# Kernel optimization log

Hardware: AMD Instinct MI355X
Metric: run time of the kernel (lower is better)

The kernel has to match this reference:

```python
import jax, jax.numpy as jnp
import numpy as np

QDEPTH = 8
WIDTH = 64
HEIGHT = 64
WIRES = 12  # ceil(log2(64*64))
BATCH = 1024


def setup_inputs() -> dict:
    key = jax.random.key(0)
    k1, k2 = jax.random.split(key)
    x = jax.random.normal(k1, (BATCH, 1, WIDTH, HEIGHT), dtype=jnp.float32)
    # torch.nn.Parameter(torch.randn(weight_shape) * 0.4)
    weights = jax.random.normal(k2, (QDEPTH, WIRES, 3), dtype=jnp.float32) * 0.4
    return {"x": x, "weights": weights, "reps": 1}


def _rot_matrices(angles):
    # angles: (L, W, 3) -> (L, W, 2, 2) complex64; Rot(phi, theta, omega) = RZ(omega) RY(theta) RZ(phi)
    phi, theta, omega = angles[..., 0], angles[..., 1], angles[..., 2]
    c = jnp.cos(theta * 0.5).astype(jnp.complex64)
    s = jnp.sin(theta * 0.5).astype(jnp.complex64)
    ep = jnp.exp(-0.5j * (phi + omega).astype(jnp.complex64))  # e^{-i(phi+omega)/2}
    em = jnp.exp(-0.5j * (phi - omega).astype(jnp.complex64))  # e^{-i(phi-omega)/2}
    row0 = jnp.stack([ep * c, -jnp.conj(em) * s], axis=-1)
    row1 = jnp.stack([em * s, jnp.conj(ep) * c], axis=-1)
    return jnp.stack([row0, row1], axis=-2)


def _apply_1q(state, U, wire):
    # state: (B, 2, 2, ..., 2); apply 2x2 U on axis wire+1
    ax = wire + 1
    s = jnp.moveaxis(state, ax, -1)
    s = s @ U.T  # out[..., i] = sum_j U[i, j] s[..., j]
    return jnp.moveaxis(s, -1, ax)


def _apply_cnot(state, control, target):
    c, t = control + 1, target + 1
    s0, s1 = jnp.split(state, 2, axis=c)   # control = 0 / 1 halves
    s1 = jnp.flip(s1, axis=t)              # X on target where control = 1
    return jnp.concatenate([s0, s1], axis=c)


def _sel_layer(state, mats_l, r):
    # one StronglyEntanglingLayers layer: Rot on every wire, then CNOT ring of range r
    for w in range(WIRES):
        state = _apply_1q(state, mats_l[w], w)
    for w in range(WIRES):
        state = _apply_cnot(state, w, (w + r) % WIRES)
    return state


def _circuit(state, weights, reps):
    mats = _rot_matrices(jnp.tanh(weights))  # qw_map.tanh applied to raw weights
    for _ in range(reps):
        for l in range(QDEPTH):
            r = (l % (WIRES - 1)) + 1  # PennyLane default ranges
            layer = jax.checkpoint(lambda s, m, _r=r: _sel_layer(s, m, _r))
            state = layer(state, mats[l])
    return state


def reference(x, weights, reps):
    b = x.shape[0]
    v = x.reshape(b, -1)  # (b, 4096)
    norm = jnp.linalg.norm(v, axis=-1, keepdims=True)
    v = (v / norm).astype(jnp.complex64)
    state = v.reshape((b,) + (2,) * WIRES)
    state = _circuit(state, weights, reps)
    out = state.reshape(b, -1) * norm
    return out.reshape(b, 1, WIDTH, HEIGHT)
```

## Files before the change

### kernel.cpp

```cpp
#include <hip/hip_runtime.h>

#define WIRES   12
#define NSTATE  4096
#define QDEPTH  8
#define BLOCK   256
#define PER_T   16

using f2 = __attribute__((ext_vector_type(2))) float;

__device__ __forceinline__ int slotf(int a) { return a + (a >> 4); }

constexpr int colF(int l, int j) {
    int rr = (l % (WIRES - 1)) + 1;
    int v = 1 << j;
    for (int k = WIRES - 1; k >= 0; --k) {
        int bc = 11 - k;
        int bt = 11 - ((k + rr) % WIRES);
        v ^= ((v >> bc) & 1) << bt;
    }
    return v;
}
struct ColsT { int v[QDEPTH][WIRES]; };
constexpr ColsT mkCols() {
    ColsT c{};
    for (int l = 0; l < QDEPTH; ++l)
        for (int j = 0; j < WIRES; ++j) c.v[l][j] = colF(l, j);
    return c;
}
static __device__ const ColsT COLS = mkCols();

__global__ void mats_kernel(const float* __restrict__ wts, f2* __restrict__ mg)
{
    int t = blockIdx.x * blockDim.x + threadIdx.x;
    if (t >= QDEPTH * WIRES) return;
    float phi   = tanhf(wts[t * 3 + 0]);
    float theta = tanhf(wts[t * 3 + 1]);
    float omega = tanhf(wts[t * 3 + 2]);
    float c  = cosf(theta * 0.5f);
    float s  = sinf(theta * 0.5f);
    float a  = 0.5f * (phi + omega);
    float bm = 0.5f * (phi - omega);
    float ca = cosf(a),  sa = sinf(a);
    float cb = cosf(bm), sb = sinf(bm);
    f2* m = mg + t * 8;
    m[0] = f2{ c * ca,  c * ca};
    m[1] = f2{ c * sa, -c * sa};
    m[2] = f2{-s * cb, -s * cb};
    m[3] = f2{ s * sb, -s * sb};
    m[4] = f2{ s * cb,  s * cb};
    m[5] = f2{ s * sb, -s * sb};
    m[6] = f2{ c * ca,  c * ca};
    m[7] = f2{-c * sa,  c * sa};
}

template<int P>
__device__ __forceinline__ void gate(f2 r[PER_T], const f2* __restrict__ m)
{
    const f2 u00r = m[0], u00w = m[1], u01r = m[2], u01w = m[3];
    const f2 u10r = m[4], u10w = m[5], u11r = m[6], u11w = m[7];
    #pragma unroll
    for (int pr = 0; pr < PER_T / 2; pr += 2) {
        const int k0 = ((pr >> P) << (P + 1)) | (pr & ((1 << P) - 1));
        const int k1 = k0 | (1 << P);
        const int q  = pr + 1;
        const int j0 = ((q >> P) << (P + 1)) | (q & ((1 << P) - 1));
        const int j1 = j0 | (1 << P);
        f2 a0, b0, a1, b1;
        asm("v_pk_mul_f32 %0, %4, %8\n\t"
            "v_pk_mul_f32 %1, %4, %12\n\t"
            "v_pk_mul_f32 %2, %6, %8\n\t"
            "v_pk_mul_f32 %3, %6, %12\n\t"
            "v_pk_fma_f32 %0, %4, %9, %0 op_sel:[1,0,0] op_sel_hi:[0,1,1]\n\t"
            "v_pk_fma_f32 %1, %4, %13, %1 op_sel:[1,0,0] op_sel_hi:[0,1,1]\n\t"
            "v_pk_fma_f32 %2, %6, %9, %2 op_sel:[1,0,0] op_sel_hi:[0,1,1]\n\t"
            "v_pk_fma_f32 %3, %6, %13, %3 op_sel:[1,0,0] op_sel_hi:[0,1,1]\n\t"
            "v_pk_fma_f32 %0, %5, %10, %0\n\t"
            "v_pk_fma_f32 %1, %5, %14, %1\n\t"
            "v_pk_fma_f32 %2, %7, %10, %2\n\t"
            "v_pk_fma_f32 %3, %7, %14, %3\n\t"
            "v_pk_fma_f32 %0, %5, %11, %0 op_sel:[1,0,0] op_sel_hi:[0,1,1]\n\t"
            "v_pk_fma_f32 %1, %5, %15, %1 op_sel:[1,0,0] op_sel_hi:[0,1,1]\n\t"
            "v_pk_fma_f32 %2, %7, %11, %2 op_sel:[1,0,0] op_sel_hi:[0,1,1]\n\t"
            "v_pk_fma_f32 %3, %7, %15, %3 op_sel:[1,0,0] op_sel_hi:[0,1,1]"
            : "=&v"(a0), "=&v"(b0), "=&v"(a1), "=&v"(b1)
            : "v"(r[k0]), "v"(r[k1]), "v"(r[j0]), "v"(r[j1]),
              "v"(u00r), "v"(u00w), "v"(u01r), "v"(u01w),
              "v"(u10r), "v"(u10w), "v"(u11r), "v"(u11w));
        r[k0] = a0; r[k1] = b0; r[j0] = a1; r[j1] = b1;
    }
}

__global__ __launch_bounds__(BLOCK, 2) void qsim_kernel(
    const float* __restrict__ x,
    const f2*    __restrict__ mats_g,
    const int*   __restrict__ reps_ptr,
    float*       __restrict__ out,
    int write_mode)
{
    __shared__ f2 st[2 * 4352];
    f2* const sA = st;
    f2* const sB = st + 4352;

    const int g   = threadIdx.x;
    const int eA  = blockIdx.x * 2;
    const int eB  = eA + 1;
    const int ghi = g >> 4, glo = g & 15;
    const int w1b = 17 * g;
    const int rb1 = 272 * ghi + glo;
    const int rb2 = 17 * ghi + glo;

    const float4* xA4 = (const float4*)(x + (size_t)eA * NSTATE) + g * 4;
    const float4* xB4 = (const float4*)(x + (size_t)eB * NSTATE) + g * 4;
    f2 rA[PER_T], rB[PER_T];
    #pragma unroll
    for (int c = 0; c < 4; ++c) {
        float4 va = xA4[c];
        rA[4*c+0] = f2{va.x, 0.f}; rA[4*c+1] = f2{va.y, 0.f};
        rA[4*c+2] = f2{va.z, 0.f}; rA[4*c+3] = f2{va.w, 0.f};
        float4 vb = xB4[c];
        rB[4*c+0] = f2{vb.x, 0.f}; rB[4*c+1] = f2{vb.y, 0.f};
        rB[4*c+2] = f2{vb.z, 0.f}; rB[4*c+3] = f2{vb.w, 0.f};
    }

    const int reps = reps_ptr[0];
    for (int rep = 0; rep < reps; ++rep) {
        #pragma unroll 1
        for (int l = 0; l < QDEPTH; ++l) {
            const f2* M = mats_g + l * WIRES * 8;

            gate<3>(rA, M + 8*8);  gate<2>(rA, M + 9*8);
            gate<1>(rA, M + 10*8); gate<0>(rA, M + 11*8);
            #pragma unroll
            for (int k = 0; k < PER_T; ++k) sA[w1b + k] = rA[k];
            gate<3>(rB, M + 8*8);  gate<2>(rB, M + 9*8);
            gate<1>(rB, M + 10*8); gate<0>(rB, M + 11*8);
            #pragma unroll
            for (int k = 0; k < PER_T; ++k) sB[w1b + k] = rB[k];
            __syncthreads();

            #pragma unroll
            for (int k = 0; k < PER_T; ++k) rA[k] = sA[rb1 + 17 * k];
            #pragma unroll
            for (int k = 0; k < PER_T; ++k) rB[k] = sB[rb1 + 17 * k];

            gate<3>(rA, M + 4*8); gate<2>(rA, M + 5*8);
            gate<1>(rA, M + 6*8); gate<0>(rA, M + 7*8);
            #pragma unroll
            for (int k = 0; k < PER_T; ++k) sA[rb1 + 17 * k] = rA[k];
            gate<3>(rB, M + 4*8); gate<2>(rB, M + 5*8);
            gate<1>(rB, M + 6*8); gate<0>(rB, M + 7*8);
            #pragma unroll
            for (int k = 0; k < PER_T; ++k) sB[rb1 + 17 * k] = rB[k];
            __syncthreads();

            #pragma unroll
            for (int k = 0; k < PER_T; ++k) rA[k] = sA[rb2 + 272 * k];
            #pragma unroll
            for (int k = 0; k < PER_T; ++k) rB[k] = sB[rb2 + 272 * k];

            gate<3>(rA, M + 0*8); gate<2>(rA, M + 1*8);
            gate<1>(rA, M + 2*8); gate<0>(rA, M + 3*8);
            #pragma unroll
            for (int k = 0; k < PER_T; ++k) sA[rb2 + 272 * k] = rA[k];
            gate<3>(rB, M + 0*8); gate<2>(rB, M + 1*8);
            gate<1>(rB, M + 2*8); gate<0>(rB, M + 3*8);
            #pragma unroll
            for (int k = 0; k < PER_T; ++k) sB[rb2 + 272 * k] = rB[k];
            __syncthreads();

            int Fg = 0;
            #pragma unroll
            for (int j = 0; j < 8; ++j)
                Fg ^= ((g >> j) & 1) ? COLS.v[l][4 + j] : 0;
            const int c0 = COLS.v[l][0], c1 = COLS.v[l][1];
            const int c2 = COLS.v[l][2], c3 = COLS.v[l][3];
            #pragma unroll
            for (int k = 0; k < PER_T; ++k) {
                int ck = ((k & 1) ? c0 : 0) ^ ((k & 2) ? c1 : 0) ^
                         ((k & 4) ? c2 : 0) ^ ((k & 8) ? c3 : 0);
                int s  = slotf(Fg ^ ck);
                rA[k] = sA[s];
                rB[k] = sB[s];
            }
            __syncthreads();
        }
    }

    if (write_mode == 0) {
        float4* oA4 = (float4*)(out + (size_t)eA * NSTATE) + g * 4;
        float4* oB4 = (float4*)(out + (size_t)eB * NSTATE) + g * 4;
        #pragma unroll
        for (int c = 0; c < 4; ++c) {
            oA4[c] = make_float4(rA[4*c].x, rA[4*c+1].x, rA[4*c+2].x, rA[4*c+3].x);
            oB4[c] = make_float4(rB[4*c].x, rB[4*c+1].x, rB[4*c+2].x, rB[4*c+3].x);
        }
    } else {
        float4* oA4 = (float4*)((float2*)out + (size_t)eA * NSTATE) + g * 8;
        float4* oB4 = (float4*)((float2*)out + (size_t)eB * NSTATE) + g * 8;
        #pragma unroll
        for (int k = 0; k < PER_T; k += 2) {
            oA4[k >> 1] = make_float4(rA[k].x, rA[k].y, rA[k+1].x, rA[k+1].y);
            oB4[k >> 1] = make_float4(rB[k].x, rB[k].y, rB[k+1].x, rB[k+1].y);
        }
    }
}

extern "C" void kernel_launch(void* const* d_in, const int* in_sizes, int n_in,
                              void* d_out, int out_size, void* d_ws, size_t ws_size,
                              hipStream_t stream) {
    const float* x    = (const float*)d_in[0];
    const float* wts  = (const float*)d_in[1];
    const int*   reps = (const int*)d_in[2];
    float*       out  = (float*)d_out;
    f2*          mg   = (f2*)d_ws;
    (void)in_sizes; (void)n_in; (void)ws_size;

    const int write_mode = (out_size >= 2 * 1024 * NSTATE) ? 1 : 0;

    mats_kernel<<<1, 128, 0, stream>>>(wts, mg);
    qsim_kernel<<<512, BLOCK, 0, stream>>>(x, mg, reps, out, write_mode);
}
```

Before: 151.0 us.

## Stagger the two state vectors' phases so LDS traffic overlaps the other's gate math

Restructures each layer so the two per-block state vectors (A and B) run offset by half a phase. While one vector does its gate arithmetic, the other's shared-memory reads and writes are issued, and B's final CNOT-permutation read is deferred into the next layer. This aims to hide LDS latency behind packed-FMA work and to give the barriers less idle time. The cost is six barriers per layer instead of four and a slightly more complex dependency chain, including a trailing read after the loop.

```diff
diff --git a/kernel.cpp b/kernel.cpp
--- a/kernel.cpp
+++ b/kernel.cpp
@@ -90,6 +90,31 @@
     }
 }
 
+template<int PH>
+__device__ __forceinline__ void gphase(f2 r[PER_T], const f2* __restrict__ M)
+{
+    const int base = (2 - PH) * 4;
+    gate<3>(r, M + (base + 0) * 8); gate<2>(r, M + (base + 1) * 8);
+    gate<1>(r, M + (base + 2) * 8); gate<0>(r, M + (base + 3) * 8);
+}
+
+__device__ __forceinline__ void fread(f2 r[PER_T], const f2* __restrict__ st,
+                                      int l, int g)
+{
+    int Fg = 0;
+    #pragma unroll
+    for (int j = 0; j < 8; ++j)
+        Fg ^= ((g >> j) & 1) ? COLS.v[l][4 + j] : 0;
+    const int c0 = COLS.v[l][0], c1 = COLS.v[l][1];
+    const int c2 = COLS.v[l][2], c3 = COLS.v[l][3];
+    #pragma unroll
+    for (int k = 0; k < PER_T; ++k) {
+        int ck = ((k & 1) ? c0 : 0) ^ ((k & 2) ? c1 : 0) ^
+                 ((k & 4) ? c2 : 0) ^ ((k & 8) ? c3 : 0);
+        r[k] = st[slotf(Fg ^ ck)];
+    }
+}
+
 __global__ __launch_bounds__(BLOCK, 2) void qsim_kernel(
     const float* __restrict__ x,
     const f2*    __restrict__ mats_g,
@@ -123,68 +148,56 @@
     }
 
     const int reps = reps_ptr[0];
+    int pl = -1;
     for (int rep = 0; rep < reps; ++rep) {
         #pragma unroll 1
         for (int l = 0; l < QDEPTH; ++l) {
             const f2* M = mats_g + l * WIRES * 8;
 
-            gate<3>(rA, M + 8*8);  gate<2>(rA, M + 9*8);
-            gate<1>(rA, M + 10*8); gate<0>(rA, M + 11*8);
+            gphase<0>(rA, M);
+            if (pl >= 0) fread(rB, sB, pl, g);
             #pragma unroll
             for (int k = 0; k < PER_T; ++k) sA[w1b + k] = rA[k];
-            gate<3>(rB, M + 8*8);  gate<2>(rB, M + 9*8);
-            gate<1>(rB, M + 10*8); gate<0>(rB, M + 11*8);
+            __syncthreads();
+
+            gphase<0>(rB, M);
+            #pragma unroll
+            for (int k = 0; k < PER_T; ++k) rA[k] = sA[rb1 + 17 * k];
             #pragma unroll
             for (int k = 0; k < PER_T; ++k) sB[w1b + k] = rB[k];
             __syncthreads();
 
-            #pragma unroll
-            for (int k = 0; k < PER_T; ++k) rA[k] = sA[rb1 + 17 * k];
+            gphase<1>(rA, M);
             #pragma unroll
             for (int k = 0; k < PER_T; ++k) rB[k] = sB[rb1 + 17 * k];
-
-            gate<3>(rA, M + 4*8); gate<2>(rA, M + 5*8);
-            gate<1>(rA, M + 6*8); gate<0>(rA, M + 7*8);
             #pragma unroll
             for (int k = 0; k < PER_T; ++k) sA[rb1 + 17 * k] = rA[k];
-            gate<3>(rB, M + 4*8); gate<2>(rB, M + 5*8);
-            gate<1>(rB, M + 6*8); gate<0>(rB, M + 7*8);
+            __syncthreads();
+
+            gphase<1>(rB, M);
+            #pragma unroll
+            for (int k = 0; k < PER_T; ++k) rA[k] = sA[rb2 + 272 * k];
             #pragma unroll
             for (int k = 0; k < PER_T; ++k) sB[rb1 + 17 * k] = rB[k];
             __syncthreads();
 
-            #pragma unroll
-            for (int k = 0; k < PER_T; ++k) rA[k] = sA[rb2 + 272 * k];
+            gphase<2>(rA, M);
             #pragma unroll
             for (int k = 0; k < PER_T; ++k) rB[k] = sB[rb2 + 272 * k];
-
-            gate<3>(rA, M + 0*8); gate<2>(rA, M + 1*8);
-            gate<1>(rA, M + 2*8); gate<0>(rA, M + 3*8);
             #pragma unroll
             for (int k = 0; k < PER_T; ++k) sA[rb2 + 272 * k] = rA[k];
-            gate<3>(rB, M + 0*8); gate<2>(rB, M + 1*8);
-            gate<1>(rB, M + 2*8); gate<0>(rB, M + 3*8);
+            __syncthreads();
+
+            gphase<2>(rB, M);
+            fread(rA, sA, l, g);
             #pragma unroll
             for (int k = 0; k < PER_T; ++k) sB[rb2 + 272 * k] = rB[k];
             __syncthreads();
 
-            int Fg = 0;
-            #pragma unroll
-            for (int j = 0; j < 8; ++j)
-                Fg ^= ((g >> j) & 1) ? COLS.v[l][4 + j] : 0;
-            const int c0 = COLS.v[l][0], c1 = COLS.v[l][1];
-            const int c2 = COLS.v[l][2], c3 = COLS.v[l][3];
-            #pragma unroll
-            for (int k = 0; k < PER_T; ++k) {
-                int ck = ((k & 1) ? c0 : 0) ^ ((k & 2) ? c1 : 0) ^
-                         ((k & 4) ? c2 : 0) ^ ((k & 8) ? c3 : 0);
-                int s  = slotf(Fg ^ ck);
-                rA[k] = sA[s];
-                rB[k] = sB[s];
-            }
-            __syncthreads();
+            pl = l;
         }
     }
+    if (pl >= 0) fread(rB, sB, pl, g);
 
     if (write_mode == 0) {
         float4* oA4 = (float4*)(out + (size_t)eA * NSTATE) + g * 4;
```

After: 151.8 us. Within noise of the previous version (+0.5%).
